# Kernel tuning notes

Hardware: AMD Instinct MI355X
Metric: run time of the kernel (lower is better)

The kernel has to match this reference:

```python
import jax, jax.numpy as jnp
import numpy as np

B, N, C = 64, 1024, 128


def setup_inputs() -> dict:
    key = jax.random.key(0)
    k1, k2, k3, k4, k5, k6 = jax.random.split(key, 6)
    adj_vals = jax.random.uniform(k1, (B, N, N), dtype=jnp.float32)
    mask = jax.random.uniform(k2, (B, N, N)) < 0.1
    adjacent = jnp.where(mask, adj_vals, 0.0)
    annotations = jax.random.normal(k3, (B, N, C), dtype=jnp.float32)
    # GraphConvolution bias, shape (1,1,C)
    gc_bias = jax.random.normal(k4, (1, 1, C), dtype=jnp.float32) * 0.05
    # Keras GRU params (reset_after=True default): kernel (C,3C), recurrent (C,3C), bias (2,3C)
    kernel = jax.random.normal(k5, (C, 3 * C), dtype=jnp.float32) / np.sqrt(C)
    recurrent_kernel = jax.random.normal(k6, (C, 3 * C), dtype=jnp.float32) / np.sqrt(C)
    gru_bias = jnp.zeros((2, 3 * C), dtype=jnp.float32)
    return {"adjacent": adjacent, "annotations": annotations, "gc_bias": gc_bias,
            "kernel": kernel, "recurrent_kernel": recurrent_kernel, "gru_bias": gru_bias}


def reference(adjacent, annotations, gc_bias, kernel, recurrent_kernel, gru_bias):
    # GraphConvolution: per-graph adj @ annotations, batched, + bias
    v = jnp.einsum('bij,bjc->bic', adjacent, annotations) + gc_bias  # [B,N,C]
    b, n, c = v.shape
    x = v.reshape(-1, c)            # visible states, one GRU step each
    h = annotations.reshape(-1, c)  # initial hidden states
    # single-step Keras GRU (reset_after=True)
    mx = x @ kernel + gru_bias[0]
    mh = h @ recurrent_kernel + gru_bias[1]
    xz, xr, xh = jnp.split(mx, 3, axis=-1)
    hz, hr, hh_in = jnp.split(mh, 3, axis=-1)
    z = jax.nn.sigmoid(xz + hz)
    r = jax.nn.sigmoid(xr + hr)
    hh = jnp.tanh(xh + r * hh_in)
    out = z * h + (1.0 - z) * hh
    return out.reshape(b, n, c)
```

## Files before the change

kernel.cpp:

```cpp
#include <hip/hip_runtime.h>

typedef unsigned short ushort_t;
typedef __attribute__((ext_vector_type(8))) short bf16x8;
typedef __attribute__((ext_vector_type(8))) unsigned short u16x8;
typedef __attribute__((ext_vector_type(4))) float f32x4;

#define B_ 64
#define N_ 1024
#define C_ 128

static __device__ __forceinline__ unsigned short f2bf(float f) {
  union { float f; unsigned int i; } v; v.f = f;
  unsigned int i = v.i;
  return (unsigned short)((i + 0x7FFFu + ((i >> 16) & 1u)) >> 16);
}
static __device__ __forceinline__ void split1(float x, ushort_t& h, ushort_t& l) {
  union { float f; unsigned int i; } u; u.f = x;
  h = (ushort_t)(u.i >> 16);
  union { unsigned int i; float f; } t; t.i = u.i & 0xFFFF0000u;
  union { float f; unsigned int i; } w; w.f = x - t.f;
  l = (ushort_t)(w.i >> 16);
}
static __device__ __forceinline__ bf16x8 as_bf(u16x8 v) {
  union { u16x8 u; bf16x8 b; } x; x.u = v; return x.b;
}
static __device__ __forceinline__ void gload_lds16(const void* g, void* l) {
  __builtin_amdgcn_global_load_lds((const __attribute__((address_space(1))) void*)g,
                                   (__attribute__((address_space(3))) void*)l,
                                   16, 0, 0);
}

__global__ __launch_bounds__(256) void tsplit(const float* __restrict__ src,
                                              ushort_t* __restrict__ dh,
                                              ushort_t* __restrict__ dl,
                                              int rows, int cols, long sb, long db) {
  __shared__ float tile[64][65];
  const int t = threadIdx.x;
  src += (long)blockIdx.z * sb;
  dh  += (long)blockIdx.z * db;
  dl  += (long)blockIdx.z * db;
  const int r0 = blockIdx.y * 64, c0 = blockIdx.x * 64;
#pragma unroll
  for (int p = 0; p < 4; ++p) {
    int row = p * 16 + (t >> 4), c4 = (t & 15) * 4;
    f32x4 v = *(const f32x4*)(src + (long)(r0 + row) * cols + c0 + c4);
#pragma unroll
    for (int j = 0; j < 4; ++j) tile[row][c4 + j] = v[j];
  }
  __syncthreads();
  const int oc = t >> 2;
#pragma unroll
  for (int p = 0; p < 2; ++p) {
    int ck = (t & 3) + p * 4;
    u16x8 vh, vl;
#pragma unroll
    for (int j = 0; j < 8; ++j) {
      ushort_t hj, lj;
      split1(tile[ck * 8 + j][oc], hj, lj);
      vh[j] = hj; vl[j] = lj;
    }
    long o = (long)(c0 + oc) * rows + r0 + ck * 8;
    *(u16x8*)(dh + o) = vh;
    *(u16x8*)(dl + o) = vl;
  }
}

__global__ __launch_bounds__(256, 2) void gc_gru(const float* __restrict__ adj,
                                                 const ushort_t* __restrict__ annTh,
                                                 const ushort_t* __restrict__ annTl,
                                                 const float* __restrict__ ann,
                                                 const float* __restrict__ gcb,
                                                 const ushort_t* __restrict__ kTh,
                                                 const ushort_t* __restrict__ kTl,
                                                 const ushort_t* __restrict__ rTh,
                                                 const float* __restrict__ gb,
                                                 float* __restrict__ out) {
  __shared__ __align__(16) float vlds[128 * 132];
  ushort_t* ldsB = (ushort_t*)vlds;

  const int tid = threadIdx.x;
  const int w = tid >> 6, lane = tid & 63;
  const int wr = w >> 1, wc = w & 1;
  const int swz = (blockIdx.x & 7) * 64 + (blockIdx.x >> 3);
  const int b = swz >> 3;
  const int m0 = (swz & 7) * 128;

  const ushort_t* aThb = annTh + (long)b * C_ * N_;
  const ushort_t* aTlb = annTl + (long)b * C_ * N_;

  const int srow8 = lane >> 3;
  const int klog  = ((lane & 7) * 16) ^ (srow8 << 4);
  const int fr = lane & 15;
  const int kg = lane >> 4;

  const float* aBase = adj + ((long)b * N_ + m0 + wr * 64 + fr) * N_ + kg * 8;

  f32x4 acc[4][4] = {};
  f32x4 Aa[8], Ab[8];

#define STAGE(CUR, T)                                                          \
  _Pragma("unroll")                                                            \
  for (int jj = 0; jj < 4; ++jj) {                                             \
    int j_ = w * 4 + jj;                                                       \
    long so_ = (long)(j_ * 8 + srow8) * N_ + (T) * 64 + (klog >> 1);           \
    gload_lds16(aThb + so_, (void*)(ldsB + ((CUR) * 2 + 0) * 8192 + j_ * 512));\
    gload_lds16(aTlb + so_, (void*)(ldsB + ((CUR) * 2 + 1) * 8192 + j_ * 512));\
  }

#define LOADA(DST, T, KK)                                                      \
  _Pragma("unroll")                                                            \
  for (int mi = 0; mi < 4; ++mi) {                                             \
    const float* g_ = aBase + (long)mi * 16 * N_ + (T) * 64 + (KK) * 32;       \
    DST[2 * mi]     = *(const f32x4*)g_;                                       \
    DST[2 * mi + 1] = *(const f32x4*)(g_ + 4);                                 \
  }

#define COMPUTE(CUR, KK, AREG)                                                 \
  {                                                                            \
    bf16x8 bh_[4], bl_[4], ah_[4], al_[4];                                     \
    _Pragma("unroll")                                                          \
    for (int ni = 0; ni < 4; ++ni) {                                           \
      int row_ = wc * 64 + ni * 16 + fr;                                       \
      int kb_ = ((KK) * 64 + kg * 16) ^ ((row_ & 7) << 4);                     \
      bh_[ni] = *(const bf16x8*)((const char*)ldsB + ((CUR) * 2 + 0) * 16384 + row_ * 128 + kb_); \
      bl_[ni] = *(const bf16x8*)((const char*)ldsB + ((CUR) * 2 + 1) * 16384 + row_ * 128 + kb_); \
    }                                                                          \
    _Pragma("unroll")                                                          \
    for (int mi = 0; mi < 4; ++mi) {                                           \
      u16x8 vh_, vl_;                                                          \
      _Pragma("unroll")                                                        \
      for (int j = 0; j < 4; ++j) {                                            \
        ushort_t hj_, lj_;                                                     \
        split1(AREG[2 * mi][j], hj_, lj_);     vh_[j] = hj_;     vl_[j] = lj_; \
        split1(AREG[2 * mi + 1][j], hj_, lj_); vh_[4 + j] = hj_; vl_[4 + j] = lj_; \
      }                                                                        \
      ah_[mi] = as_bf(vh_); al_[mi] = as_bf(vl_);                              \
    }                                                                          \
    _Pragma("unroll")                                                          \
    for (int mi = 0; mi < 4; ++mi)                                             \
      _Pragma("unroll")                                                        \
      for (int ni = 0; ni < 4; ++ni) {                                         \
        acc[mi][ni] = __builtin_amdgcn_mfma_f32_16x16x32_bf16(ah_[mi], bh_[ni], acc[mi][ni], 0, 0, 0); \
        acc[mi][ni] = __builtin_amdgcn_mfma_f32_16x16x32_bf16(al_[mi], bh_[ni], acc[mi][ni], 0, 0, 0); \
        acc[mi][ni] = __builtin_amdgcn_mfma_f32_16x16x32_bf16(ah_[mi], bl_[ni], acc[mi][ni], 0, 0, 0); \
      }                                                                        \
  }

  STAGE(0, 0)
  LOADA(Aa, 0, 0)
  LOADA(Ab, 0, 1)
  __syncthreads();

#pragma unroll 1
  for (int t = 0; t < 15; ++t) {
    const int cur = t & 1;
    STAGE(cur ^ 1, t + 1)
    COMPUTE(cur, 0, Aa)
    LOADA(Aa, t + 1, 0)
    COMPUTE(cur, 1, Ab)
    LOADA(Ab, t + 1, 1)
    __syncthreads();
  }
  COMPUTE(1, 0, Aa)
  COMPUTE(1, 1, Ab)
  __syncthreads();

#undef STAGE
#undef LOADA
#undef COMPUTE

#pragma unroll
  for (int ni = 0; ni < 4; ++ni) {
    int col = wc * 64 + ni * 16 + fr;
    float bias = gcb[col];
#pragma unroll
    for (int mi = 0; mi < 4; ++mi) {
      int row = wr * 64 + mi * 16 + kg * 4;
#pragma unroll
      for (int r = 0; r < 4; ++r)
        vlds[(row + r) * 132 + col] = acc[mi][ni][r] + bias;
    }
  }
  __syncthreads();

  const long grow = (long)b * N_ + m0 + w * 32;

  bf16x8 xh[2][4], xl[2][4], hh[2][4];
#pragma unroll
  for (int s = 0; s < 2; ++s)
#pragma unroll
    for (int kk = 0; kk < 4; ++kk) {
      int lrow = w * 32 + s * 16 + fr;
      int k0 = kk * 32 + kg * 8;
      f32x4 x0 = *(const f32x4*)&vlds[lrow * 132 + k0];
      f32x4 x1 = *(const f32x4*)&vlds[lrow * 132 + k0 + 4];
      u16x8 th, tl;
#pragma unroll
      for (int j = 0; j < 4; ++j) {
        ushort_t hj, lj;
        split1(x0[j], hj, lj); th[j] = hj; tl[j] = lj;
        split1(x1[j], hj, lj); th[4 + j] = hj; tl[4 + j] = lj;
      }
      xh[s][kk] = as_bf(th); xl[s][kk] = as_bf(tl);
      const float* hrow = ann + (grow + s * 16 + fr) * C_ + k0;
      f32x4 h0 = *(const f32x4*)hrow;
      f32x4 h1 = *(const f32x4*)(hrow + 4);
      u16x8 hv;
#pragma unroll
      for (int j = 0; j < 4; ++j) { hv[j] = f2bf(h0[j]); hv[4 + j] = f2bf(h1[j]); }
      hh[s][kk] = as_bf(hv);
    }

#define GATE(G, AK0, AK1, AR0, AR1)                                                         \
  do {                                                                                      \
    const ushort_t* kh_ = kTh + (long)((G) * C_ + cb) * C_;                                 \
    const ushort_t* kl_ = kTl + (long)((G) * C_ + cb) * C_;                                 \
    const ushort_t* rh_ = rTh + (long)((G) * C_ + cb) * C_;                                 \
    bf16x8 KH[4], KL[4], RH[4];                                                             \
    _Pragma("unroll")                                                                       \
    for (int kk = 0; kk < 4; ++kk) {                                                        \
      int o_ = kk * 32 + kg * 8;                                                            \
      KH[kk] = *(const bf16x8*)(kh_ + o_);                                                  \
      KL[kk] = *(const bf16x8*)(kl_ + o_);                                                  \
      RH[kk] = *(const bf16x8*)(rh_ + o_);                                                  \
    }                                                                                       \
    _Pragma("unroll")                                                                       \
    for (int kk = 0; kk < 4; ++kk) {                                                        \
      AK0 = __builtin_amdgcn_mfma_f32_16x16x32_bf16(xh[0][kk], KH[kk], AK0, 0, 0, 0);       \
      AK1 = __builtin_amdgcn_mfma_f32_16x16x32_bf16(xh[1][kk], KH[kk], AK1, 0, 0, 0);       \
      AK0 = __builtin_amdgcn_mfma_f32_16x16x32_bf16(xl[0][kk], KH[kk], AK0, 0, 0, 0);       \
      AK1 = __builtin_amdgcn_mfma_f32_16x16x32_bf16(xl[1][kk], KH[kk], AK1, 0, 0, 0);       \
      AK0 = __builtin_amdgcn_mfma_f32_16x16x32_bf16(xh[0][kk], KL[kk], AK0, 0, 0, 0);       \
      AK1 = __builtin_amdgcn_mfma_f32_16x16x32_bf16(xh[1][kk], KL[kk], AK1, 0, 0, 0);       \
    }                                                                                       \
    _Pragma("unroll")                                                                       \
    for (int kk = 0; kk < 4; ++kk) {                                                        \
      AR0 = __builtin_amdgcn_mfma_f32_16x16x32_bf16(hh[0][kk], RH[kk], AR0, 0, 0, 0);       \
      AR1 = __builtin_amdgcn_mfma_f32_16x16x32_bf16(hh[1][kk], RH[kk], AR1, 0, 0, 0);       \
    }                                                                                       \
  } while (0)

#pragma unroll 1
  for (int n = 0; n < 8; ++n) {
    const int cb = n * 16 + fr;
    f32x4 az0 = {}, az1 = {}, ar0 = {}, ar1 = {}, ax0 = {}, ax1 = {}, ah0 = {}, ah1 = {};
    GATE(0, az0, az1, az0, az1);
    GATE(1, ar0, ar1, ar0, ar1);
    GATE(2, ax0, ax1, ah0, ah1);

    const float bz  = gb[cb] + gb[384 + cb];
    const float brr = gb[128 + cb] + gb[384 + 128 + cb];
    const float bxh = gb[256 + cb];
    const float bhi = gb[384 + 256 + cb];
#pragma unroll
    for (int s = 0; s < 2; ++s) {
      const f32x4& az_ = s ? az1 : az0;
      const f32x4& ar_ = s ? ar1 : ar0;
      const f32x4& ax_ = s ? ax1 : ax0;
      const f32x4& ah_ = s ? ah1 : ah0;
#pragma unroll
      for (int r = 0; r < 4; ++r) {
        long row = grow + s * 16 + kg * 4 + r;
        float hval = ann[row * C_ + cb];
        float zz = 1.f / (1.f + __expf(-(az_[r] + bz)));
        float rr = 1.f / (1.f + __expf(-(ar_[r] + brr)));
        float hpre = ax_[r] + bxh + rr * (ah_[r] + bhi);
        hpre = fminf(fmaxf(hpre, -15.f), 15.f);
        float e2 = __expf(2.f * hpre);
        float th = (e2 - 1.f) / (e2 + 1.f);
        out[row * C_ + cb] = zz * hval + (1.f - zz) * th;
      }
    }
  }
#undef GATE
}

extern "C" void kernel_launch(void* const* d_in, const int* in_sizes, int n_in,
                              void* d_out, int out_size, void* d_ws, size_t ws_size,
                              hipStream_t stream) {
  const float* adj = (const float*)d_in[0];
  const float* ann = (const float*)d_in[1];
  const float* gcb = (const float*)d_in[2];
  const float* ker = (const float*)d_in[3];
  const float* rk  = (const float*)d_in[4];
  const float* gb  = (const float*)d_in[5];
  float* out = (float*)d_out;

  char* ws = (char*)d_ws;
  ushort_t* annTh = (ushort_t*)(ws);
  ushort_t* annTl = (ushort_t*)(ws + 16777216);
  ushort_t* kTh   = (ushort_t*)(ws + 33554432);
  ushort_t* kTl   = (ushort_t*)(ws + 33652736);
  ushort_t* rTh   = (ushort_t*)(ws + 33751040);
  ushort_t* rTl   = (ushort_t*)(ws + 33849344);

  hipLaunchKernelGGL(tsplit, dim3(2, 16, 64), dim3(256), 0, stream,
                     ann, annTh, annTl, 1024, 128, (long)1024 * 128, (long)128 * 1024);
  hipLaunchKernelGGL(tsplit, dim3(6, 2, 1), dim3(256), 0, stream,
                     ker, kTh, kTl, 128, 384, 0L, 0L);
  hipLaunchKernelGGL(tsplit, dim3(6, 2, 1), dim3(256), 0, stream,
                     rk, rTh, rTl, 128, 384, 0L, 0L);
  hipLaunchKernelGGL(gc_gru, dim3(512), dim3(256), 0, stream,
                     adj, annTh, annTl, ann, gcb, kTh, kTl, rTh, gb, out);
}
```

Measured before the change: 181.1 us.

## Use 512-thread blocks with smaller per-wave tiles and single A register buffer

The fused graph-conv + GRU kernel now runs 8 waves per block (4x2 wave grid) instead of 4. Each wave computes a 64x32 tile instead of 64x64 and keeps one A register buffer instead of two, so A prefetch is no longer pipelined across iterations. LDS shrinks to 64KB and the epilogue hands tiles over in two passes through a shared buffer, with each wave handling 16 rows in the GRU stage. The goal is to cut registers per wave and raise occupancy to hide latency, at the cost of losing register double-buffering of the adjacency loads and adding extra barriers.

```diff
diff --git a/kernel.cpp b/kernel.cpp
--- a/kernel.cpp
+++ b/kernel.cpp
@@ -65,7 +65,7 @@
   }
 }
 
-__global__ __launch_bounds__(256, 2) void gc_gru(const float* __restrict__ adj,
+__global__ __launch_bounds__(512, 4) void gc_gru(const float* __restrict__ adj,
                                                  const ushort_t* __restrict__ annTh,
                                                  const ushort_t* __restrict__ annTl,
                                                  const float* __restrict__ ann,
@@ -75,12 +75,12 @@
                                                  const ushort_t* __restrict__ rTh,
                                                  const float* __restrict__ gb,
                                                  float* __restrict__ out) {
-  __shared__ __align__(16) float vlds[128 * 132];
-  ushort_t* ldsB = (ushort_t*)vlds;
+  __shared__ __align__(16) ushort_t lds[4 * 8192];
+  float* hbuf = (float*)lds;
 
   const int tid = threadIdx.x;
   const int w = tid >> 6, lane = tid & 63;
-  const int wr = w >> 1, wc = w & 1;
+  const int wr = w >> 2, wc = w & 3;
   const int swz = (blockIdx.x & 7) * 64 + (blockIdx.x >> 3);
   const int b = swz >> 3;
   const int m0 = (swz & 7) * 128;
@@ -95,123 +95,128 @@
 
   const float* aBase = adj + ((long)b * N_ + m0 + wr * 64 + fr) * N_ + kg * 8;
 
-  f32x4 acc[4][4] = {};
-  f32x4 Aa[8], Ab[8];
-
-#define STAGE(CUR, T)                                                          \
-  _Pragma("unroll")                                                            \
-  for (int jj = 0; jj < 4; ++jj) {                                             \
-    int j_ = w * 4 + jj;                                                       \
-    long so_ = (long)(j_ * 8 + srow8) * N_ + (T) * 64 + (klog >> 1);           \
-    gload_lds16(aThb + so_, (void*)(ldsB + ((CUR) * 2 + 0) * 8192 + j_ * 512));\
-    gload_lds16(aTlb + so_, (void*)(ldsB + ((CUR) * 2 + 1) * 8192 + j_ * 512));\
-  }
-
-#define LOADA(DST, T, KK)                                                      \
-  _Pragma("unroll")                                                            \
-  for (int mi = 0; mi < 4; ++mi) {                                             \
-    const float* g_ = aBase + (long)mi * 16 * N_ + (T) * 64 + (KK) * 32;       \
-    DST[2 * mi]     = *(const f32x4*)g_;                                       \
-    DST[2 * mi + 1] = *(const f32x4*)(g_ + 4);                                 \
-  }
-
-#define COMPUTE(CUR, KK, AREG)                                                 \
-  {                                                                            \
-    bf16x8 bh_[4], bl_[4], ah_[4], al_[4];                                     \
-    _Pragma("unroll")                                                          \
-    for (int ni = 0; ni < 4; ++ni) {                                           \
-      int row_ = wc * 64 + ni * 16 + fr;                                       \
-      int kb_ = ((KK) * 64 + kg * 16) ^ ((row_ & 7) << 4);                     \
-      bh_[ni] = *(const bf16x8*)((const char*)ldsB + ((CUR) * 2 + 0) * 16384 + row_ * 128 + kb_); \
-      bl_[ni] = *(const bf16x8*)((const char*)ldsB + ((CUR) * 2 + 1) * 16384 + row_ * 128 + kb_); \
-    }                                                                          \
-    _Pragma("unroll")                                                          \
-    for (int mi = 0; mi < 4; ++mi) {                                           \
-      u16x8 vh_, vl_;                                                          \
-      _Pragma("unroll")                                                        \
-      for (int j = 0; j < 4; ++j) {                                            \
-        ushort_t hj_, lj_;                                                     \
-        split1(AREG[2 * mi][j], hj_, lj_);     vh_[j] = hj_;     vl_[j] = lj_; \
-        split1(AREG[2 * mi + 1][j], hj_, lj_); vh_[4 + j] = hj_; vl_[4 + j] = lj_; \
-      }                                                                        \
-      ah_[mi] = as_bf(vh_); al_[mi] = as_bf(vl_);                              \
-    }                                                                          \
-    _Pragma("unroll")                                                          \
-    for (int mi = 0; mi < 4; ++mi)                                             \
-      _Pragma("unroll")                                                        \
-      for (int ni = 0; ni < 4; ++ni) {                                         \
+  f32x4 acc[4][2] = {};
+  f32x4 A[8];
+
+#define STAGE(CUR, T)                                                            \
+  _Pragma("unroll")                                                              \
+  for (int jj = 0; jj < 2; ++jj) {                                               \
+    int j_ = w * 2 + jj;                                                         \
+    long so_ = (long)(j_ * 8 + srow8) * N_ + (T) * 64 + (klog >> 1);             \
+    gload_lds16(aThb + so_, (void*)(lds + ((CUR) * 2 + 0) * 8192 + j_ * 512));   \
+    gload_lds16(aTlb + so_, (void*)(lds + ((CUR) * 2 + 1) * 8192 + j_ * 512));   \
+  }
+
+#define LOADA(T, KK)                                                             \
+  _Pragma("unroll")                                                              \
+  for (int mi = 0; mi < 4; ++mi) {                                               \
+    const float* g_ = aBase + (long)mi * 16 * N_ + (T) * 64 + (KK) * 32;         \
+    A[2 * mi]     = *(const f32x4*)g_;                                           \
+    A[2 * mi + 1] = *(const f32x4*)(g_ + 4);                                     \
+  }
+
+#define COMPUTE(CUR, KK)                                                         \
+  {                                                                              \
+    bf16x8 bh_[2], bl_[2], ah_[4], al_[4];                                       \
+    _Pragma("unroll")                                                            \
+    for (int ni = 0; ni < 2; ++ni) {                                             \
+      int row_ = wc * 32 + ni * 16 + fr;                                         \
+      int kb_ = ((KK) * 64 + kg * 16) ^ ((row_ & 7) << 4);                       \
+      bh_[ni] = *(const bf16x8*)((const char*)lds + ((CUR) * 2 + 0) * 16384 + row_ * 128 + kb_); \
+      bl_[ni] = *(const bf16x8*)((const char*)lds + ((CUR) * 2 + 1) * 16384 + row_ * 128 + kb_); \
+    }                                                                            \
+    _Pragma("unroll")                                                            \
+    for (int mi = 0; mi < 4; ++mi) {                                             \
+      u16x8 vh_, vl_;                                                            \
+      _Pragma("unroll")                                                          \
+      for (int j = 0; j < 4; ++j) {                                              \
+        ushort_t hj_, lj_;                                                       \
+        split1(A[2 * mi][j], hj_, lj_);     vh_[j] = hj_;     vl_[j] = lj_;      \
+        split1(A[2 * mi + 1][j], hj_, lj_); vh_[4 + j] = hj_; vl_[4 + j] = lj_;  \
+      }                                                                          \
+      ah_[mi] = as_bf(vh_); al_[mi] = as_bf(vl_);                                \
+    }                                                                            \
+    _Pragma("unroll")                                                            \
+    for (int mi = 0; mi < 4; ++mi)                                               \
+      _Pragma("unroll")                                                          \
+      for (int ni = 0; ni < 2; ++ni) {                                           \
         acc[mi][ni] = __builtin_amdgcn_mfma_f32_16x16x32_bf16(ah_[mi], bh_[ni], acc[mi][ni], 0, 0, 0); \
         acc[mi][ni] = __builtin_amdgcn_mfma_f32_16x16x32_bf16(al_[mi], bh_[ni], acc[mi][ni], 0, 0, 0); \
         acc[mi][ni] = __builtin_amdgcn_mfma_f32_16x16x32_bf16(ah_[mi], bl_[ni], acc[mi][ni], 0, 0, 0); \
-      }                                                                        \
+      }                                                                          \
   }
 
   STAGE(0, 0)
-  LOADA(Aa, 0, 0)
-  LOADA(Ab, 0, 1)
   __syncthreads();
 
 #pragma unroll 1
-  for (int t = 0; t < 15; ++t) {
+  for (int t = 0; t < 16; ++t) {
     const int cur = t & 1;
-    STAGE(cur ^ 1, t + 1)
-    COMPUTE(cur, 0, Aa)
-    LOADA(Aa, t + 1, 0)
-    COMPUTE(cur, 1, Ab)
-    LOADA(Ab, t + 1, 1)
+    if (t < 15) { STAGE(cur ^ 1, t + 1) }
+    LOADA(t, 0)
+    COMPUTE(cur, 0)
+    LOADA(t, 1)
+    COMPUTE(cur, 1)
     __syncthreads();
   }
-  COMPUTE(1, 0, Aa)
-  COMPUTE(1, 1, Ab)
-  __syncthreads();
 
 #undef STAGE
 #undef LOADA
 #undef COMPUTE
 
-#pragma unroll
-  for (int ni = 0; ni < 4; ++ni) {
-    int col = wc * 64 + ni * 16 + fr;
-    float bias = gcb[col];
-#pragma unroll
-    for (int mi = 0; mi < 4; ++mi) {
-      int row = wr * 64 + mi * 16 + kg * 4;
-#pragma unroll
-      for (int r = 0; r < 4; ++r)
-        vlds[(row + r) * 132 + col] = acc[mi][ni][r] + bias;
-    }
-  }
-  __syncthreads();
-
-  const long grow = (long)b * N_ + m0 + w * 32;
-
-  bf16x8 xh[2][4], xl[2][4], hh[2][4];
-#pragma unroll
-  for (int s = 0; s < 2; ++s)
-#pragma unroll
-    for (int kk = 0; kk < 4; ++kk) {
-      int lrow = w * 32 + s * 16 + fr;
-      int k0 = kk * 32 + kg * 8;
-      f32x4 x0 = *(const f32x4*)&vlds[lrow * 132 + k0];
-      f32x4 x1 = *(const f32x4*)&vlds[lrow * 132 + k0 + 4];
-      u16x8 th, tl;
-#pragma unroll
-      for (int j = 0; j < 4; ++j) {
-        ushort_t hj, lj;
-        split1(x0[j], hj, lj); th[j] = hj; tl[j] = lj;
-        split1(x1[j], hj, lj); th[4 + j] = hj; tl[4 + j] = lj;
+  const long grow = (long)b * N_ + m0 + w * 16;
+
+  bf16x8 hh[4];
+#pragma unroll
+  for (int kk = 0; kk < 4; ++kk) {
+    const float* hrow = ann + (grow + fr) * C_ + kk * 32 + kg * 8;
+    f32x4 h0 = *(const f32x4*)hrow;
+    f32x4 h1 = *(const f32x4*)(hrow + 4);
+    u16x8 hv;
+#pragma unroll
+    for (int j = 0; j < 4; ++j) { hv[j] = f2bf(h0[j]); hv[4 + j] = f2bf(h1[j]); }
+    hh[kk] = as_bf(hv);
+  }
+
+  bf16x8 xh[4], xl[4];
+#pragma unroll 1
+  for (int p = 0; p < 2; ++p) {
+    if (wr == p) {
+#pragma unroll
+      for (int ni = 0; ni < 2; ++ni) {
+        int col = wc * 32 + ni * 16 + fr;
+        float bias = gcb[col];
+#pragma unroll
+        for (int mi = 0; mi < 4; ++mi) {
+          int lrow = mi * 16 + kg * 4;
+#pragma unroll
+          for (int r = 0; r < 4; ++r)
+            hbuf[(lrow + r) * 132 + col] = acc[mi][ni][r] + bias;
+        }
       }
-      xh[s][kk] = as_bf(th); xl[s][kk] = as_bf(tl);
-      const float* hrow = ann + (grow + s * 16 + fr) * C_ + k0;
-      f32x4 h0 = *(const f32x4*)hrow;
-      f32x4 h1 = *(const f32x4*)(hrow + 4);
-      u16x8 hv;
-#pragma unroll
-      for (int j = 0; j < 4; ++j) { hv[j] = f2bf(h0[j]); hv[4 + j] = f2bf(h1[j]); }
-      hh[s][kk] = as_bf(hv);
-    }
-
-#define GATE(G, AK0, AK1, AR0, AR1)                                                         \
+    }
+    __syncthreads();
+    if (wr == p) {
+#pragma unroll
+      for (int kk = 0; kk < 4; ++kk) {
+        int lrow = (w & 3) * 16 + fr;
+        int k0 = kk * 32 + kg * 8;
+        f32x4 x0 = *(const f32x4*)&hbuf[lrow * 132 + k0];
+        f32x4 x1 = *(const f32x4*)&hbuf[lrow * 132 + k0 + 4];
+        u16x8 th, tl;
+#pragma unroll
+        for (int j = 0; j < 4; ++j) {
+          ushort_t hj, lj;
+          split1(x0[j], hj, lj); th[j] = hj; tl[j] = lj;
+          split1(x1[j], hj, lj); th[4 + j] = hj; tl[4 + j] = lj;
+        }
+        xh[kk] = as_bf(th); xl[kk] = as_bf(tl);
+      }
+    }
+    __syncthreads();
+  }
+
+#define GATE(G, AK, AR)                                                                     \
   do {                                                                                      \
     const ushort_t* kh_ = kTh + (long)((G) * C_ + cb) * C_;                                 \
     const ushort_t* kl_ = kTl + (long)((G) * C_ + cb) * C_;                                 \
@@ -226,50 +231,39 @@
     }                                                                                       \
     _Pragma("unroll")                                                                       \
     for (int kk = 0; kk < 4; ++kk) {                                                        \
-      AK0 = __builtin_amdgcn_mfma_f32_16x16x32_bf16(xh[0][kk], KH[kk], AK0, 0, 0, 0);       \
-      AK1 = __builtin_amdgcn_mfma_f32_16x16x32_bf16(xh[1][kk], KH[kk], AK1, 0, 0, 0);       \
-      AK0 = __builtin_amdgcn_mfma_f32_16x16x32_bf16(xl[0][kk], KH[kk], AK0, 0, 0, 0);       \
-      AK1 = __builtin_amdgcn_mfma_f32_16x16x32_bf16(xl[1][kk], KH[kk], AK1, 0, 0, 0);       \
-      AK0 = __builtin_amdgcn_mfma_f32_16x16x32_bf16(xh[0][kk], KL[kk], AK0, 0, 0, 0);       \
-      AK1 = __builtin_amdgcn_mfma_f32_16x16x32_bf16(xh[1][kk], KL[kk], AK1, 0, 0, 0);       \
+      AK = __builtin_amdgcn_mfma_f32_16x16x32_bf16(xh[kk], KH[kk], AK, 0, 0, 0);            \
+      AK = __builtin_amdgcn_mfma_f32_16x16x32_bf16(xl[kk], KH[kk], AK, 0, 0, 0);            \
+      AK = __builtin_amdgcn_mfma_f32_16x16x32_bf16(xh[kk], KL[kk], AK, 0, 0, 0);            \
     }                                                                                       \
     _Pragma("unroll")                                                                       \
     for (int kk = 0; kk < 4; ++kk) {                                                        \
-      AR0 = __builtin_amdgcn_mfma_f32_16x16x32_bf16(hh[0][kk], RH[kk], AR0, 0, 0, 0);       \
-      AR1 = __builtin_amdgcn_mfma_f32_16x16x32_bf16(hh[1][kk], RH[kk], AR1, 0, 0, 0);       \
+      AR = __builtin_amdgcn_mfma_f32_16x16x32_bf16(hh[kk], RH[kk], AR, 0, 0, 0);            \
     }                                                                                       \
   } while (0)
 
 #pragma unroll 1
   for (int n = 0; n < 8; ++n) {
     const int cb = n * 16 + fr;
-    f32x4 az0 = {}, az1 = {}, ar0 = {}, ar1 = {}, ax0 = {}, ax1 = {}, ah0 = {}, ah1 = {};
-    GATE(0, az0, az1, az0, az1);
-    GATE(1, ar0, ar1, ar0, ar1);
-    GATE(2, ax0, ax1, ah0, ah1);
+    f32x4 az = {}, ar = {}, ax = {}, ah = {};
+    GATE(0, az, az);
+    GATE(1, ar, ar);
+    GATE(2, ax, ah);
 
     const float bz  = gb[cb] + gb[384 + cb];
     const float brr = gb[128 + cb] + gb[384 + 128 + cb];
     const float bxh = gb[256 + cb];
     const float bhi = gb[384 + 256 + cb];
 #pragma unroll
-    for (int s = 0; s < 2; ++s) {
-      const f32x4& az_ = s ? az1 : az0;
-      const f32x4& ar_ = s ? ar1 : ar0;
-      const f32x4& ax_ = s ? ax1 : ax0;
-      const f32x4& ah_ = s ? ah1 : ah0;
-#pragma unroll
-      for (int r = 0; r < 4; ++r) {
-        long row = grow + s * 16 + kg * 4 + r;
-        float hval = ann[row * C_ + cb];
-        float zz = 1.f / (1.f + __expf(-(az_[r] + bz)));
-        float rr = 1.f / (1.f + __expf(-(ar_[r] + brr)));
-        float hpre = ax_[r] + bxh + rr * (ah_[r] + bhi);
-        hpre = fminf(fmaxf(hpre, -15.f), 15.f);
-        float e2 = __expf(2.f * hpre);
-        float th = (e2 - 1.f) / (e2 + 1.f);
-        out[row * C_ + cb] = zz * hval + (1.f - zz) * th;
-      }
+    for (int r = 0; r < 4; ++r) {
+      long row = grow + kg * 4 + r;
+      float hval = ann[row * C_ + cb];
+      float zz = 1.f / (1.f + __expf(-(az[r] + bz)));
+      float rr = 1.f / (1.f + __expf(-(ar[r] + brr)));
+      float hpre = ax[r] + bxh + rr * (ah[r] + bhi);
+      hpre = fminf(fmaxf(hpre, -15.f), 15.f);
+      float e2 = __expf(2.f * hpre);
+      float th = (e2 - 1.f) / (e2 + 1.f);
+      out[row * C_ + cb] = zz * hval + (1.f - zz) * th;
     }
   }
 #undef GATE
@@ -300,6 +294,6 @@
                      ker, kTh, kTl, 128, 384, 0L, 0L);
   hipLaunchKernelGGL(tsplit, dim3(6, 2, 1), dim3(256), 0, stream,
                      rk, rTh, rTl, 128, 384, 0L, 0L);
-  hipLaunchKernelGGL(gc_gru, dim3(512), dim3(256), 0, stream,
+  hipLaunchKernelGGL(gc_gru, dim3(512), dim3(512), 0, stream,
                      adj, annTh, annTl, ann, gcb, kTh, kTl, rTh, gb, out);
 }
```

New measurement: 282.5 us. 56.0% more time.

## Stage adjacency tiles through LDS with async loads and vmcnt-based barriers

Applied to the files above, without the earlier changes.

The fp32 adjacency A-tile is now brought into LDS with global_load_lds alongside the split bf16 annotation tiles, instead of being loaded into registers per wave. The K step shrinks from 64 to 32 so two stages fit in the shared buffer, and each gets swizzled layouts for A and B. The __syncthreads calls become hand-written s_waitcnt vmcnt(8)/lgkmcnt(0) plus s_barrier so the next stage's loads stay in flight during compute. This cuts register pressure and global-to-register latency, but doubles the barrier count and relies on the inline-asm wait counts matching the number of outstanding loads.

```diff
diff --git a/kernel.cpp b/kernel.cpp
--- a/kernel.cpp
+++ b/kernel.cpp
@@ -29,6 +29,9 @@
                                    (__attribute__((address_space(3))) void*)l,
                                    16, 0, 0);
 }
+
+#define PIPE_BAR(N) asm volatile("s_waitcnt vmcnt(" #N ")\n\ts_barrier" ::: "memory")
+#define POST_BAR()  asm volatile("s_waitcnt lgkmcnt(0)\n\ts_barrier" ::: "memory")
 
 __global__ __launch_bounds__(256) void tsplit(const float* __restrict__ src,
                                               ushort_t* __restrict__ dh,
@@ -76,7 +79,7 @@
                                                  const float* __restrict__ gb,
                                                  float* __restrict__ out) {
   __shared__ __align__(16) float vlds[128 * 132];
-  ushort_t* ldsB = (ushort_t*)vlds;
+  float* lds_all = vlds;
 
   const int tid = threadIdx.x;
   const int w = tid >> 6, lane = tid & 63;
@@ -85,54 +88,66 @@
   const int b = swz >> 3;
   const int m0 = (swz & 7) * 128;
 
+  const float*    adjb = adj   + ((long)b * N_ + m0) * N_;
   const ushort_t* aThb = annTh + (long)b * C_ * N_;
   const ushort_t* aTlb = annTl + (long)b * C_ * N_;
 
-  const int srow8 = lane >> 3;
-  const int klog  = ((lane & 7) * 16) ^ (srow8 << 4);
   const int fr = lane & 15;
   const int kg = lane >> 4;
 
-  const float* aBase = adj + ((long)b * N_ + m0 + wr * 64 + fr) * N_ + kg * 8;
+  const int aRow = lane >> 3;
+  const int aCs  = (lane & 7) ^ aRow;
+  const int bRow = lane >> 2;
+  const int bCs  = (lane & 3) ^ ((lane >> 3) & 3);
 
   f32x4 acc[4][4] = {};
-  f32x4 Aa[8], Ab[8];
-
-#define STAGE(CUR, T)                                                          \
-  _Pragma("unroll")                                                            \
-  for (int jj = 0; jj < 4; ++jj) {                                             \
-    int j_ = w * 4 + jj;                                                       \
-    long so_ = (long)(j_ * 8 + srow8) * N_ + (T) * 64 + (klog >> 1);           \
-    gload_lds16(aThb + so_, (void*)(ldsB + ((CUR) * 2 + 0) * 8192 + j_ * 512));\
-    gload_lds16(aTlb + so_, (void*)(ldsB + ((CUR) * 2 + 1) * 8192 + j_ * 512));\
-  }
-
-#define LOADA(DST, T, KK)                                                      \
-  _Pragma("unroll")                                                            \
-  for (int mi = 0; mi < 4; ++mi) {                                             \
-    const float* g_ = aBase + (long)mi * 16 * N_ + (T) * 64 + (KK) * 32;       \
-    DST[2 * mi]     = *(const f32x4*)g_;                                       \
-    DST[2 * mi + 1] = *(const f32x4*)(g_ + 4);                                 \
-  }
-
-#define COMPUTE(CUR, KK, AREG)                                                 \
+
+#define STAGE(Q, T)                                                            \
   {                                                                            \
+    const int k0_ = (T) * 32;                                                  \
+    float*    A_  = lds_all + (Q) * 8192;                                      \
+    ushort_t* Bh_ = (ushort_t*)(lds_all + (Q) * 8192 + 4096);                  \
+    ushort_t* Bl_ = (ushort_t*)(lds_all + (Q) * 8192 + 6144);                  \
+    _Pragma("unroll")                                                          \
+    for (int jj = 0; jj < 4; ++jj) {                                           \
+      int j_ = w * 4 + jj;                                                     \
+      gload_lds16(adjb + (long)(j_ * 8 + aRow) * N_ + k0_ + aCs * 4,           \
+                  (void*)(A_ + j_ * 256));                                     \
+    }                                                                          \
+    _Pragma("unroll")                                                          \
+    for (int jj = 0; jj < 2; ++jj) {                                           \
+      int j_ = w * 2 + jj;                                                     \
+      long so_ = (long)(j_ * 16 + bRow) * N_ + k0_ + bCs * 8;                  \
+      gload_lds16(aThb + so_, (void*)(Bh_ + j_ * 512));                        \
+      gload_lds16(aTlb + so_, (void*)(Bl_ + j_ * 512));                        \
+    }                                                                          \
+  }
+
+#define COMPUTE(Q)                                                             \
+  {                                                                            \
+    const float*    A_  = lds_all + (Q) * 8192;                                \
+    const ushort_t* Bh_ = (const ushort_t*)(lds_all + (Q) * 8192 + 4096);      \
+    const ushort_t* Bl_ = (const ushort_t*)(lds_all + (Q) * 8192 + 6144);      \
     bf16x8 bh_[4], bl_[4], ah_[4], al_[4];                                     \
     _Pragma("unroll")                                                          \
     for (int ni = 0; ni < 4; ++ni) {                                           \
       int row_ = wc * 64 + ni * 16 + fr;                                       \
-      int kb_ = ((KK) * 64 + kg * 16) ^ ((row_ & 7) << 4);                     \
-      bh_[ni] = *(const bf16x8*)((const char*)ldsB + ((CUR) * 2 + 0) * 16384 + row_ * 128 + kb_); \
-      bl_[ni] = *(const bf16x8*)((const char*)ldsB + ((CUR) * 2 + 1) * 16384 + row_ * 128 + kb_); \
+      int kb_ = (kg << 4) ^ ((((row_) >> 1) & 3) << 4);                        \
+      bh_[ni] = *(const bf16x8*)((const char*)Bh_ + row_ * 64 + kb_);          \
+      bl_[ni] = *(const bf16x8*)((const char*)Bl_ + row_ * 64 + kb_);          \
     }                                                                          \
     _Pragma("unroll")                                                          \
     for (int mi = 0; mi < 4; ++mi) {                                           \
+      int row_ = wr * 64 + mi * 16 + fr;                                       \
+      int b0_ = row_ * 128 + ((kg * 32) ^ ((row_ & 7) << 4));                  \
+      f32x4 a0_ = *(const f32x4*)((const char*)A_ + b0_);                      \
+      f32x4 a1_ = *(const f32x4*)((const char*)A_ + (b0_ ^ 16));               \
       u16x8 vh_, vl_;                                                          \
       _Pragma("unroll")                                                        \
       for (int j = 0; j < 4; ++j) {                                            \
         ushort_t hj_, lj_;                                                     \
-        split1(AREG[2 * mi][j], hj_, lj_);     vh_[j] = hj_;     vl_[j] = lj_; \
-        split1(AREG[2 * mi + 1][j], hj_, lj_); vh_[4 + j] = hj_; vl_[4 + j] = lj_; \
+        split1(a0_[j], hj_, lj_); vh_[j] = hj_;     vl_[j] = lj_;              \
+        split1(a1_[j], hj_, lj_); vh_[4 + j] = hj_; vl_[4 + j] = lj_;          \
       }                                                                        \
       ah_[mi] = as_bf(vh_); al_[mi] = as_bf(vl_);                              \
     }                                                                          \
@@ -147,26 +162,20 @@
   }
 
   STAGE(0, 0)
-  LOADA(Aa, 0, 0)
-  LOADA(Ab, 0, 1)
-  __syncthreads();
 
 #pragma unroll 1
-  for (int t = 0; t < 15; ++t) {
+  for (int t = 0; t < 31; ++t) {
     const int cur = t & 1;
     STAGE(cur ^ 1, t + 1)
-    COMPUTE(cur, 0, Aa)
-    LOADA(Aa, t + 1, 0)
-    COMPUTE(cur, 1, Ab)
-    LOADA(Ab, t + 1, 1)
-    __syncthreads();
-  }
-  COMPUTE(1, 0, Aa)
-  COMPUTE(1, 1, Ab)
+    PIPE_BAR(8);
+    COMPUTE(cur)
+    POST_BAR();
+  }
+  PIPE_BAR(0);
+  COMPUTE(1)
   __syncthreads();
 
 #undef STAGE
-#undef LOADA
 #undef COMPUTE
 
 #pragma unroll
@@ -190,10 +199,9 @@
   for (int s = 0; s < 2; ++s)
 #pragma unroll
     for (int kk = 0; kk < 4; ++kk) {
-      int lrow = w * 32 + s * 16 + fr;
-      int k0 = kk * 32 + kg * 8;
-      f32x4 x0 = *(const f32x4*)&vlds[lrow * 132 + k0];
-      f32x4 x1 = *(const f32x4*)&vlds[lrow * 132 + k0 + 4];
+      int lo = (w * 32 + s * 16 + fr) * 132 + kk * 32 + kg * 8;
+      f32x4 x0 = *(const f32x4*)&vlds[lo];
+      f32x4 x1 = *(const f32x4*)&vlds[lo + 4];
       u16x8 th, tl;
 #pragma unroll
       for (int j = 0; j < 4; ++j) {
@@ -202,7 +210,7 @@
         split1(x1[j], hj, lj); th[4 + j] = hj; tl[4 + j] = lj;
       }
       xh[s][kk] = as_bf(th); xl[s][kk] = as_bf(tl);
-      const float* hrow = ann + (grow + s * 16 + fr) * C_ + k0;
+      const float* hrow = ann + (grow + s * 16 + fr) * C_ + kk * 32 + kg * 8;
       f32x4 h0 = *(const f32x4*)hrow;
       f32x4 h1 = *(const f32x4*)(hrow + 4);
       u16x8 hv;
```

Result: faster. 163.8 us (-9.5%).
